# Performance work log

Hardware: AMD Instinct MI355X
Metric: run time of the kernel (lower is better)

The kernel has to match this reference:

```python
import jax, jax.numpy as jnp
import numpy as np

B, L1, Q_DIM, V_DIM = 4, 4096, 256, 256
NH, NL, NP = 8, 4, 4
LEVELS = [(128, 128), (64, 64), (32, 32), (16, 16)]
L2 = sum(h * w for h, w in LEVELS)  # 21760


def setup_inputs() -> dict:
    key = jax.random.key(0)
    ks = jax.random.split(key, 12)
    xav = lambda k, so, si: jax.random.normal(k, (so, si), jnp.float32) * np.sqrt(2.0 / (so + si)).astype(np.float32)
    # reference windows: centers in [0.1,0.9], box sizes in [0.05,0.25]
    c = 0.1 + 0.8 * jax.random.uniform(ks[0], (B, L1, 2), jnp.float32)
    s = 0.05 + 0.2 * jax.random.uniform(ks[1], (B, L1, 2), jnp.float32)
    v_shape = jnp.array(LEVELS, dtype=jnp.int32)
    v_start_index = jnp.array(np.cumsum([0] + [h * w for h, w in LEVELS[:-1]]), dtype=jnp.int32)
    return {
        'query': jax.random.normal(ks[2], (B, L1, Q_DIM), jnp.float32),
        'value': jax.random.normal(ks[3], (B, L2, V_DIM), jnp.float32),
        'v_shape': v_shape,
        'v_mask': jnp.zeros((B, L2), jnp.bool_),
        'v_start_index': v_start_index,
        'v_valid_ratios': jnp.ones((B, 1, 1, NL, 1, 2), jnp.float32),
        'ref_windows': jnp.concatenate([c, s], axis=-1),
        'Wo': 0.01 * jax.random.normal(ks[4], (NH * NL * NP * 2, Q_DIM), jnp.float32),
        'bo': 0.5 * jax.random.normal(ks[5], (NH * NL * NP * 2,), jnp.float32),
        'Wa': 0.02 * jax.random.normal(ks[6], (NH * NL * NP, Q_DIM), jnp.float32),
        'ba': jnp.zeros((NH * NL * NP,), jnp.float32),
        'Wv': xav(ks[7], V_DIM, V_DIM),
        'bv': jnp.zeros((V_DIM,), jnp.float32),
        'Wout': xav(ks[8], Q_DIM, V_DIM),
        'bout': jnp.zeros((Q_DIM,), jnp.float32),
    }


def _ms_deform_sample(value, v_shape, v_start, loc):
    """value: (b,l2,h,d); loc: (b,l1,h,L,P,2) in [0,1] -> (b,l1,L,P,h,d).
    Bilinear sampling with zero padding, align_corners=False semantics."""
    b, l2, h, d = value.shape
    _, l1, _, L, P, _ = loc.shape
    Hi = v_shape[:, 0][None, None, None, :, None]  # (1,1,1,L,1) int
    Wi = v_shape[:, 1][None, None, None, :, None]
    x = loc[..., 0] * Wi.astype(loc.dtype) - 0.5  # (b,l1,h,L,P)
    y = loc[..., 1] * Hi.astype(loc.dtype) - 0.5
    x0 = jnp.floor(x)
    y0 = jnp.floor(y)
    lx, ly = x - x0, y - y0
    x0i = x0.astype(jnp.int32)
    y0i = y0.astype(jnp.int32)
    start = v_start[None, None, None, :, None]
    acc = jnp.zeros((b, l1 * L * P, h, d), loc.dtype)
    for dy, wy in ((0, 1.0 - ly), (1, ly)):
        for dx, wx in ((0, 1.0 - lx), (1, lx)):
            xi = x0i + dx
            yi = y0i + dy
            valid = (xi >= 0) & (xi < Wi) & (yi >= 0) & (yi < Hi)
            w = wx * wy * valid.astype(loc.dtype)  # (b,l1,h,L,P)
            xc = jnp.clip(xi, 0, Wi - 1)
            yc = jnp.clip(yi, 0, Hi - 1)
            flat = start + yc * Wi + xc  # (b,l1,h,L,P) index into l2
            flat_t = flat.transpose(0, 1, 3, 4, 2).reshape(b, l1 * L * P, h)
            w_t = w.transpose(0, 1, 3, 4, 2).reshape(b, l1 * L * P, h)
            g = jnp.take_along_axis(value, flat_t[..., None], axis=1)  # (b,M,h,d)
            acc = acc + g * w_t[..., None]
    return acc.reshape(b, l1, L, P, h, d)


def reference(query, value, v_shape, v_mask, v_start_index, v_valid_ratios, ref_windows,
              Wo, bo, Wa, ba, Wv, bv, Wout, bout):
    b, l1, _ = query.shape
    l2 = value.shape[1]
    hd = value.shape[-1] // NH
    v = value @ Wv.T + bv
    v = jnp.where(v_mask[..., None], 0.0, v).reshape(b, l2, NH, hd)
    off = (query @ Wo.T + bo).reshape(b, l1, NH, NL, NP, 2)
    attn = jax.nn.softmax((query @ Wa.T + ba).reshape(b, l1, NH, NL * NP), axis=-1)
    attn = attn.reshape(b, l1, NH, NL, NP)
    loc = ref_windows[:, :, None, None, None, :2] + off / 8.0 * ref_windows[:, :, None, None, None, 2:]
    loc = loc * v_valid_ratios
    sampled = _ms_deform_sample(v, v_shape, v_start_index, loc)  # (b,l1,L,P,h,d)
    out = jnp.einsum('blLPhd,blhLP->blhd', sampled, attn).reshape(b, l1, NH * hd)
    out = out @ Wout.T + bout
    return out, attn
```

## Files before the change

kernel.cpp:

```cpp
#include <hip/hip_runtime.h>
#include <cstdint>
#include <cstddef>


#define L2_LEN 21760
#define BQ_TOT 16384

typedef __attribute__((ext_vector_type(8))) _Float16 half8;
typedef __attribute__((ext_vector_type(4))) float    f32x4;

__device__ __forceinline__ void glds16(const _Float16* g, _Float16* l) {
    __builtin_amdgcn_global_load_lds(
        (const __attribute__((address_space(1))) void*)g,
        (__attribute__((address_space(3))) void*)l, 16, 0, 0);
}
__device__ __forceinline__ half8 cvt8(float4 a, float4 b) {
    half8 h;
    h[0] = (_Float16)a.x; h[1] = (_Float16)a.y;
    h[2] = (_Float16)a.z; h[3] = (_Float16)a.w;
    h[4] = (_Float16)b.x; h[5] = (_Float16)b.y;
    h[6] = (_Float16)b.z; h[7] = (_Float16)b.w;
    return h;
}

__global__ __launch_bounds__(256) void cvt_weights(
    const float* __restrict__ Wv, const float* __restrict__ Wo,
    const float* __restrict__ Wa, const float* __restrict__ Wout,
    const float* __restrict__ bv, const float* __restrict__ bo,
    const float* __restrict__ ba, const float* __restrict__ bout,
    _Float16* __restrict__ Wp, float* __restrict__ bp)
{
    const int gid = blockIdx.x * 256 + threadIdx.x;
    const float* src; int off8;
    if      (gid <  8192) { src = Wv;   off8 = gid;         }
    else if (gid < 16384) { src = Wo;   off8 = gid -  8192; }
    else if (gid < 20480) { src = Wa;   off8 = gid - 16384; }
    else                  { src = Wout; off8 = gid - 20480; }
    const float4 f0 = ((const float4*)src)[off8 * 2];
    const float4 f1 = ((const float4*)src)[off8 * 2 + 1];
    ((half8*)Wp)[gid] = cvt8(f0, f1);
    if (gid < 896) {
        float b;
        if      (gid < 256) b = bv[gid];
        else if (gid < 512) b = bo[gid - 256];
        else if (gid < 640) b = ba[gid - 512];
        else                b = bout[gid - 640];
        bp[gid] = b;
    }
}

__global__ __launch_bounds__(512) void gemm_vproj(
    const float* __restrict__ A,
    const _Float16* __restrict__ Wp,
    const float* __restrict__ bp,
    _Float16* __restrict__ vh,
    const unsigned char* __restrict__ mask)
{
    __shared__ _Float16 As[4096];
    __shared__ _Float16 Bs[8192];

    const int t = threadIdx.x, lane = t & 63, wid = t >> 6;
    const int wm = wid >> 2, wn = wid & 3;
    const int bm = blockIdx.x;

    const int ar = t >> 2, akp = t & 3;
    const float* Ag = A + (size_t)(bm * 128 + ar) * 256 + akp * 8;
    _Float16* Ad = &As[((ar >> 4) * 64 + akp * 16 + (ar & 15)) * 8];

    const int u0 = wid * 128 + lane, u1 = u0 + 64;
    const int br0 = ((u0 >> 6) << 4) + (u0 & 15), bk0 = ((u0 >> 4) & 3) * 8;
    const int br1 = ((u1 >> 6) << 4) + (u1 & 15), bk1 = ((u1 >> 4) & 3) * 8;
    const _Float16* Wg0 = Wp + (size_t)br0 * 256 + bk0;
    const _Float16* Wg1 = Wp + (size_t)br1 * 256 + bk1;
    _Float16* Bd0 = &Bs[(size_t)wid * 1024];
    _Float16* Bd1 = Bd0 + 512;

    f32x4 acc[4][4] = {};

    for (int kk = 0; kk < 256; kk += 32) {
        const float4 a0 = *(const float4*)(Ag + kk);
        const float4 a1 = *(const float4*)(Ag + kk + 4);
        __syncthreads();
        glds16(Wg0 + kk, Bd0);
        glds16(Wg1 + kk, Bd1);
        *(half8*)Ad = cvt8(a0, a1);
        __syncthreads();
        half8 ah[4], bh[4];
#pragma unroll
        for (int x = 0; x < 4; ++x) {
            ah[x] = ((const half8*)As)[(wm * 4 + x) * 64 + lane];
            bh[x] = ((const half8*)Bs)[(wn * 4 + x) * 64 + lane];
        }
#pragma unroll
        for (int m = 0; m < 4; ++m)
#pragma unroll
            for (int n = 0; n < 4; ++n)
                acc[m][n] = __builtin_amdgcn_mfma_f32_16x16x32_f16(
                    ah[m], bh[n], acc[m][n], 0, 0, 0);
    }

    const int b = bm / 170;
    const int l2b = (bm - b * 170) * 128;
    const int cl = lane & 15, rl = (lane >> 4) * 4;
#pragma unroll
    for (int m = 0; m < 4; ++m) {
        const int ro = wm * 64 + m * 16 + rl;
        float mz[4];
#pragma unroll
        for (int r = 0; r < 4; ++r)
            mz[r] = mask[bm * 128 + ro + r] ? 0.0f : 1.0f;
#pragma unroll
        for (int n = 0; n < 4; ++n) {
            const int col = wn * 64 + n * 16 + cl;
            const int h = col >> 5, c = col & 31;
            const float bb = bp[col];
            _Float16* dst = vh + ((size_t)(b * 8 + h) * L2_LEN + l2b + ro) * 32 + c;
#pragma unroll
            for (int r = 0; r < 4; ++r)
                dst[(size_t)r * 32] = (_Float16)((acc[m][n][r] + bb) * mz[r]);
        }
    }
}

template<bool A_F32>
__global__ __launch_bounds__(256) void gemm_qo(
    const void* __restrict__ Av, const _Float16* __restrict__ Wp,
    const float* __restrict__ bp, int wrow0,
    float* __restrict__ C, int ldC)
{
    __shared__ _Float16 As[4096];
    __shared__ _Float16 Bs[4096];

    const int t = threadIdx.x, lane = t & 63, wid = t >> 6;
    const int wm = wid >> 1, wn = wid & 1;
    const int bm = blockIdx.x, bn = blockIdx.y;

    const int u0 = wid * 128 + lane, u1 = u0 + 64;
    const int br0 = ((u0 >> 6) << 4) + (u0 & 15), bk0 = ((u0 >> 4) & 3) * 8;
    const int br1 = ((u1 >> 6) << 4) + (u1 & 15), bk1 = ((u1 >> 4) & 3) * 8;
    const _Float16* Wg0 = Wp + (size_t)(wrow0 + bn * 128 + br0) * 256 + bk0;
    const _Float16* Wg1 = Wp + (size_t)(wrow0 + bn * 128 + br1) * 256 + bk1;
    _Float16* Bd0 = &Bs[(size_t)wid * 1024];
    _Float16* Bd1 = Bd0 + 512;

    const float*    Agf = nullptr; _Float16* Adf0 = nullptr; _Float16* Adf1 = nullptr;
    const _Float16* Agh0 = nullptr; const _Float16* Agh1 = nullptr;
    _Float16* Adh0 = nullptr; _Float16* Adh1 = nullptr;
    if (A_F32) {
        const int r = t >> 1, kp = (t & 1) * 2;
        Agf  = (const float*)Av + (size_t)(bm * 128 + r) * 256 + kp * 8;
        Adf0 = &As[((r >> 4) * 64 + kp * 16 + (r & 15)) * 8];
        Adf1 = Adf0 + 128;
    } else {
        Agh0 = (const _Float16*)Av + (size_t)(bm * 128 + br0) * 256 + bk0;
        Agh1 = (const _Float16*)Av + (size_t)(bm * 128 + br1) * 256 + bk1;
        Adh0 = &As[(size_t)wid * 1024];
        Adh1 = Adh0 + 512;
    }

    f32x4 acc[4][4] = {};

    for (int kk = 0; kk < 256; kk += 32) {
        float4 a0, a1, a2, a3;
        if (A_F32) {
            a0 = *(const float4*)(Agf + kk);      a1 = *(const float4*)(Agf + kk + 4);
            a2 = *(const float4*)(Agf + kk + 8);  a3 = *(const float4*)(Agf + kk + 12);
        }
        __syncthreads();
        glds16(Wg0 + kk, Bd0);
        glds16(Wg1 + kk, Bd1);
        if (A_F32) {
            *(half8*)Adf0 = cvt8(a0, a1);
            *(half8*)Adf1 = cvt8(a2, a3);
        } else {
            glds16(Agh0 + kk, Adh0);
            glds16(Agh1 + kk, Adh1);
        }
        __syncthreads();
        half8 ah[4], bh[4];
#pragma unroll
        for (int x = 0; x < 4; ++x) {
            ah[x] = ((const half8*)As)[(wm * 4 + x) * 64 + lane];
            bh[x] = ((const half8*)Bs)[(wn * 4 + x) * 64 + lane];
        }
#pragma unroll
        for (int m = 0; m < 4; ++m)
#pragma unroll
            for (int n = 0; n < 4; ++n)
                acc[m][n] = __builtin_amdgcn_mfma_f32_16x16x32_f16(
                    ah[m], bh[n], acc[m][n], 0, 0, 0);
    }

    const int rb = bm * 128 + wm * 64, cb = bn * 128 + wn * 64;
    const int cl = lane & 15, rl = (lane >> 4) * 4;
#pragma unroll
    for (int n = 0; n < 4; ++n) {
        const float bb = bp[wrow0 + cb + n * 16 + cl];
#pragma unroll
        for (int m = 0; m < 4; ++m)
#pragma unroll
            for (int r = 0; r < 4; ++r)
                C[(size_t)(rb + m * 16 + rl + r) * ldC + cb + n * 16 + cl] =
                    acc[m][n][r] + bb;
    }
}

__global__ __launch_bounds__(128) void sample_fused(
    const _Float16* __restrict__ v,
    const float* __restrict__ qp,
    const float* __restrict__ ref,
    const float* __restrict__ vr,
    float* __restrict__ attn_out,
    _Float16* __restrict__ sout)
{
    constexpr int HH[4] = {128, 64, 32, 16};
    constexpr int SS[4] = {0, 16384, 20480, 21504};

    const int t  = threadIdx.x;
    const int q  = blockIdx.x * 4 + (t >> 5);
    const int h  = (t >> 2) & 7;
    const int c0 = (t & 3) * 8;
    const int b  = q >> 12;

    const float* lg = qp + (size_t)q * 384 + 256 + h * 16;
    const float4 l0 = ((const float4*)lg)[0], l1 = ((const float4*)lg)[1];
    const float4 l2 = ((const float4*)lg)[2], l3 = ((const float4*)lg)[3];
    float ap[16] = {l0.x, l0.y, l0.z, l0.w, l1.x, l1.y, l1.z, l1.w,
                    l2.x, l2.y, l2.z, l2.w, l3.x, l3.y, l3.z, l3.w};
    float mx = ap[0];
#pragma unroll
    for (int j = 1; j < 16; ++j) mx = fmaxf(mx, ap[j]);
    float sum = 0.0f;
#pragma unroll
    for (int j = 0; j < 16; ++j) { ap[j] = __expf(ap[j] - mx); sum += ap[j]; }
    const float inv = 1.0f / sum;
#pragma unroll
    for (int j = 0; j < 16; ++j) ap[j] *= inv;
    if (c0 == 0) {
        float4* ao = (float4*)(attn_out + ((size_t)q * 8 + h) * 16);
        ao[0] = make_float4(ap[0], ap[1], ap[2], ap[3]);
        ao[1] = make_float4(ap[4], ap[5], ap[6], ap[7]);
        ao[2] = make_float4(ap[8], ap[9], ap[10], ap[11]);
        ao[3] = make_float4(ap[12], ap[13], ap[14], ap[15]);
    }

    const float4 rw = *(const float4*)(ref + (size_t)q * 4);
    const float* op = qp + (size_t)q * 384 + h * 32;

    float acc[8] = {};

#pragma unroll
    for (int l = 0; l < 4; ++l) {
        const int HW = HH[l];
        const float fHW = (float)HW;
        const float vrx = vr[(b * 4 + l) * 2 + 0];
        const float vry = vr[(b * 4 + l) * 2 + 1];
        const _Float16* vb = v + ((size_t)(b * 8 + h) * L2_LEN + SS[l]) * 32 + c0;
#pragma unroll
        for (int p = 0; p < 4; ++p) {
            const float a  = ap[l * 4 + p];
            const float ox = op[(l * 4 + p) * 2 + 0];
            const float oy = op[(l * 4 + p) * 2 + 1];
            const float x = (rw.x + ox * 0.125f * rw.z) * vrx * fHW - 0.5f;
            const float y = (rw.y + oy * 0.125f * rw.w) * vry * fHW - 0.5f;
            const float x0f = floorf(x), y0f = floorf(y);
            const float fx = x - x0f, fy = y - y0f;
            const int x0 = (int)x0f, y0 = (int)y0f;
            const float wx0 = (x0 >= 0 && x0 < HW)         ? (1.0f - fx) : 0.0f;
            const float wx1 = (x0 + 1 >= 0 && x0 + 1 < HW) ? fx          : 0.0f;
            const float wy0 = (y0 >= 0 && y0 < HW)         ? (1.0f - fy) : 0.0f;
            const float wy1 = (y0 + 1 >= 0 && y0 + 1 < HW) ? fy          : 0.0f;
            const int xc0 = min(max(x0, 0), HW - 1), xc1 = min(max(x0 + 1, 0), HW - 1);
            const int yc0 = min(max(y0, 0), HW - 1), yc1 = min(max(y0 + 1, 0), HW - 1);
            const float w00 = wx0 * wy0 * a, w01 = wx1 * wy0 * a;
            const float w10 = wx0 * wy1 * a, w11 = wx1 * wy1 * a;
            const half8 g00 = *(const half8*)(vb + (size_t)(yc0 * HW + xc0) * 32);
            const half8 g01 = *(const half8*)(vb + (size_t)(yc0 * HW + xc1) * 32);
            const half8 g10 = *(const half8*)(vb + (size_t)(yc1 * HW + xc0) * 32);
            const half8 g11 = *(const half8*)(vb + (size_t)(yc1 * HW + xc1) * 32);
#pragma unroll
            for (int j = 0; j < 8; ++j)
                acc[j] += w00 * (float)g00[j] + w01 * (float)g01[j]
                        + w10 * (float)g10[j] + w11 * (float)g11[j];
        }
    }

    half8 o;
#pragma unroll
    for (int j = 0; j < 8; ++j) o[j] = (_Float16)acc[j];
    *(half8*)(sout + (size_t)q * 256 + h * 32 + c0) = o;
}

extern "C" void kernel_launch(void* const* d_in, const int* in_sizes, int n_in,
                              void* d_out, int out_size, void* d_ws, size_t ws_size,
                              hipStream_t stream)
{
    const float*         query    = (const float*)d_in[0];
    const float*         value    = (const float*)d_in[1];
    const unsigned char* v_mask   = (const unsigned char*)d_in[3];
    const float*         v_ratios = (const float*)d_in[5];
    const float*         ref_w    = (const float*)d_in[6];
    const float*         Wo       = (const float*)d_in[7];
    const float*         bo       = (const float*)d_in[8];
    const float*         Wa       = (const float*)d_in[9];
    const float*         ba       = (const float*)d_in[10];
    const float*         Wv       = (const float*)d_in[11];
    const float*         bv       = (const float*)d_in[12];
    const float*         Wout     = (const float*)d_in[13];
    const float*         bout     = (const float*)d_in[14];

    float* out      = (float*)d_out;
    float* attn_out = out + (size_t)BQ_TOT * 256;

    _Float16* Wp = (_Float16*)d_ws;
    float*    bp = (float*)(Wp + 896 * 256);
    float*    qp = bp + 896;
    _Float16* vh = (_Float16*)(qp + (size_t)BQ_TOT * 384);
    _Float16* Sf = vh + (size_t)4 * L2_LEN * 256;

    cvt_weights<<<112, 256, 0, stream>>>(Wv, Wo, Wa, Wout, bv, bo, ba, bout, Wp, bp);
    gemm_vproj<<<680, 512, 0, stream>>>(value, Wp, bp, vh, v_mask);
    gemm_qo<true><<<dim3(128, 3), 256, 0, stream>>>(query, Wp, bp, 256, qp, 384);
    sample_fused<<<4096, 128, 0, stream>>>(vh, qp, ref_w, v_ratios, attn_out, Sf);
    gemm_qo<false><<<dim3(128, 2), 256, 0, stream>>>(Sf, Wp, bp, 640, out, 256);
}
```

Before: 274.5 us.

## Double-buffer GEMMs, drop weight pre-conversion, repartition sampling by level with fdot2

The separate weight-conversion kernel is removed. GEMMs now read fp32 weights and convert them while staging to shared memory. All GEMMs become register-prefetched, double-buffered loops with XOR-swizzled LDS layouts, swapped MFMA operands for vectorized epilogue stores, and 2-D grids for the value projection. The sampling kernel now assigns one level per lane instead of one channel slice, loads full 32-channel rows, and accumulates with packed fp16 dot products. Results are combined across lanes with shuffles. This lowers bilinear weight precision to fp16 and raises register pressure.

```diff
diff --git a/kernel.cpp b/kernel.cpp
--- a/kernel.cpp
+++ b/kernel.cpp
@@ -7,6 +7,8 @@
 #define BQ_TOT 16384
 
 typedef __attribute__((ext_vector_type(8))) _Float16 half8;
+typedef __attribute__((ext_vector_type(4))) _Float16 half4;
+typedef __attribute__((ext_vector_type(2))) _Float16 half2v;
 typedef __attribute__((ext_vector_type(4))) float    f32x4;
 
 __device__ __forceinline__ void glds16(const _Float16* g, _Float16* l) {
@@ -22,186 +24,201 @@
     h[6] = (_Float16)b.z; h[7] = (_Float16)b.w;
     return h;
 }
-
-__global__ __launch_bounds__(256) void cvt_weights(
-    const float* __restrict__ Wv, const float* __restrict__ Wo,
-    const float* __restrict__ Wa, const float* __restrict__ Wout,
-    const float* __restrict__ bv, const float* __restrict__ bo,
-    const float* __restrict__ ba, const float* __restrict__ bout,
-    _Float16* __restrict__ Wp, float* __restrict__ bp)
+__device__ __forceinline__ int swz_chunk(int c) {
+    const int frag = c >> 6, r = (c >> 2) & 15, k = c & 3;
+    return (frag * 64 + ((k * 16 + r) ^ (k << 2))) * 8;
+}
+
+__global__ __launch_bounds__(256, 3) void gemm_vproj(
+    const float* __restrict__ A, const float* __restrict__ Wv,
+    const float* __restrict__ bv, const unsigned char* __restrict__ mask,
+    _Float16* __restrict__ vh)
 {
-    const int gid = blockIdx.x * 256 + threadIdx.x;
-    const float* src; int off8;
-    if      (gid <  8192) { src = Wv;   off8 = gid;         }
-    else if (gid < 16384) { src = Wo;   off8 = gid -  8192; }
-    else if (gid < 20480) { src = Wa;   off8 = gid - 16384; }
-    else                  { src = Wout; off8 = gid - 20480; }
-    const float4 f0 = ((const float4*)src)[off8 * 2];
-    const float4 f1 = ((const float4*)src)[off8 * 2 + 1];
-    ((half8*)Wp)[gid] = cvt8(f0, f1);
-    if (gid < 896) {
-        float b;
-        if      (gid < 256) b = bv[gid];
-        else if (gid < 512) b = bo[gid - 256];
-        else if (gid < 640) b = ba[gid - 512];
-        else                b = bout[gid - 640];
-        bp[gid] = b;
-    }
-}
-
-__global__ __launch_bounds__(512) void gemm_vproj(
-    const float* __restrict__ A,
-    const _Float16* __restrict__ Wp,
-    const float* __restrict__ bp,
-    _Float16* __restrict__ vh,
-    const unsigned char* __restrict__ mask)
-{
-    __shared__ _Float16 As[4096];
-    __shared__ _Float16 Bs[8192];
-
-    const int t = threadIdx.x, lane = t & 63, wid = t >> 6;
-    const int wm = wid >> 2, wn = wid & 3;
-    const int bm = blockIdx.x;
-
-    const int ar = t >> 2, akp = t & 3;
-    const float* Ag = A + (size_t)(bm * 128 + ar) * 256 + akp * 8;
-    _Float16* Ad = &As[((ar >> 4) * 64 + akp * 16 + (ar & 15)) * 8];
-
-    const int u0 = wid * 128 + lane, u1 = u0 + 64;
-    const int br0 = ((u0 >> 6) << 4) + (u0 & 15), bk0 = ((u0 >> 4) & 3) * 8;
-    const int br1 = ((u1 >> 6) << 4) + (u1 & 15), bk1 = ((u1 >> 4) & 3) * 8;
-    const _Float16* Wg0 = Wp + (size_t)br0 * 256 + bk0;
-    const _Float16* Wg1 = Wp + (size_t)br1 * 256 + bk1;
-    _Float16* Bd0 = &Bs[(size_t)wid * 1024];
-    _Float16* Bd1 = Bd0 + 512;
-
-    f32x4 acc[4][4] = {};
-
-    for (int kk = 0; kk < 256; kk += 32) {
-        const float4 a0 = *(const float4*)(Ag + kk);
-        const float4 a1 = *(const float4*)(Ag + kk + 4);
-        __syncthreads();
-        glds16(Wg0 + kk, Bd0);
-        glds16(Wg1 + kk, Bd1);
-        *(half8*)Ad = cvt8(a0, a1);
-        __syncthreads();
-        half8 ah[4], bh[4];
-#pragma unroll
-        for (int x = 0; x < 4; ++x) {
-            ah[x] = ((const half8*)As)[(wm * 4 + x) * 64 + lane];
-            bh[x] = ((const half8*)Bs)[(wn * 4 + x) * 64 + lane];
-        }
-#pragma unroll
-        for (int m = 0; m < 4; ++m)
-#pragma unroll
-            for (int n = 0; n < 4; ++n)
-                acc[m][n] = __builtin_amdgcn_mfma_f32_16x16x32_f16(
-                    ah[m], bh[n], acc[m][n], 0, 0, 0);
-    }
-
-    const int b = bm / 170;
-    const int l2b = (bm - b * 170) * 128;
-    const int cl = lane & 15, rl = (lane >> 4) * 4;
-#pragma unroll
-    for (int m = 0; m < 4; ++m) {
-        const int ro = wm * 64 + m * 16 + rl;
-        float mz[4];
-#pragma unroll
-        for (int r = 0; r < 4; ++r)
-            mz[r] = mask[bm * 128 + ro + r] ? 0.0f : 1.0f;
-#pragma unroll
-        for (int n = 0; n < 4; ++n) {
-            const int col = wn * 64 + n * 16 + cl;
-            const int h = col >> 5, c = col & 31;
-            const float bb = bp[col];
-            _Float16* dst = vh + ((size_t)(b * 8 + h) * L2_LEN + l2b + ro) * 32 + c;
-#pragma unroll
-            for (int r = 0; r < 4; ++r)
-                dst[(size_t)r * 32] = (_Float16)((acc[m][n][r] + bb) * mz[r]);
-        }
-    }
-}
-
-template<bool A_F32>
-__global__ __launch_bounds__(256) void gemm_qo(
-    const void* __restrict__ Av, const _Float16* __restrict__ Wp,
-    const float* __restrict__ bp, int wrow0,
-    float* __restrict__ C, int ldC)
-{
-    __shared__ _Float16 As[4096];
-    __shared__ _Float16 Bs[4096];
+    __shared__ _Float16 As[2][4096];
+    __shared__ _Float16 Bs[2][4096];
 
     const int t = threadIdx.x, lane = t & 63, wid = t >> 6;
     const int wm = wid >> 1, wn = wid & 1;
     const int bm = blockIdx.x, bn = blockIdx.y;
 
-    const int u0 = wid * 128 + lane, u1 = u0 + 64;
-    const int br0 = ((u0 >> 6) << 4) + (u0 & 15), bk0 = ((u0 >> 4) & 3) * 8;
-    const int br1 = ((u1 >> 6) << 4) + (u1 & 15), bk1 = ((u1 >> 4) & 3) * 8;
-    const _Float16* Wg0 = Wp + (size_t)(wrow0 + bn * 128 + br0) * 256 + bk0;
-    const _Float16* Wg1 = Wp + (size_t)(wrow0 + bn * 128 + br1) * 256 + bk1;
-    _Float16* Bd0 = &Bs[(size_t)wid * 1024];
-    _Float16* Bd1 = Bd0 + 512;
-
-    const float*    Agf = nullptr; _Float16* Adf0 = nullptr; _Float16* Adf1 = nullptr;
-    const _Float16* Agh0 = nullptr; const _Float16* Agh1 = nullptr;
-    _Float16* Adh0 = nullptr; _Float16* Adh1 = nullptr;
-    if (A_F32) {
-        const int r = t >> 1, kp = (t & 1) * 2;
-        Agf  = (const float*)Av + (size_t)(bm * 128 + r) * 256 + kp * 8;
-        Adf0 = &As[((r >> 4) * 64 + kp * 16 + (r & 15)) * 8];
-        Adf1 = Adf0 + 128;
-    } else {
-        Agh0 = (const _Float16*)Av + (size_t)(bm * 128 + br0) * 256 + bk0;
-        Agh1 = (const _Float16*)Av + (size_t)(bm * 128 + br1) * 256 + bk1;
-        Adh0 = &As[(size_t)wid * 1024];
-        Adh1 = Adh0 + 512;
-    }
+    const int r0 = t >> 2, kg = (t & 3) * 8;
+    const float* Ag0 = A  + ((size_t)(bm * 128) + r0) * 256 + kg;
+    const float* Ag1 = Ag0 + (size_t)64 * 256;
+    const float* Bg0 = Wv + ((size_t)(bn * 128) + r0) * 256 + kg;
+    const float* Bg1 = Bg0 + (size_t)64 * 256;
+    const int d0 = swz_chunk(t), d1 = swz_chunk(t + 256);
+    const int rsw = (lane ^ ((lane >> 4) << 2)) * 8;
 
     f32x4 acc[4][4] = {};
-
-    for (int kk = 0; kk < 256; kk += 32) {
-        float4 a0, a1, a2, a3;
-        if (A_F32) {
-            a0 = *(const float4*)(Agf + kk);      a1 = *(const float4*)(Agf + kk + 4);
-            a2 = *(const float4*)(Agf + kk + 8);  a3 = *(const float4*)(Agf + kk + 12);
-        }
-        __syncthreads();
-        glds16(Wg0 + kk, Bd0);
-        glds16(Wg1 + kk, Bd1);
-        if (A_F32) {
-            *(half8*)Adf0 = cvt8(a0, a1);
-            *(half8*)Adf1 = cvt8(a2, a3);
-        } else {
-            glds16(Agh0 + kk, Adh0);
-            glds16(Agh1 + kk, Adh1);
-        }
-        __syncthreads();
+    float4 pa0, pa1, pa2, pa3, pb0, pb1, pb2, pb3;
+
+    pa0 = *(const float4*)Ag0; pa1 = *(const float4*)(Ag0 + 4);
+    pa2 = *(const float4*)Ag1; pa3 = *(const float4*)(Ag1 + 4);
+    pb0 = *(const float4*)Bg0; pb1 = *(const float4*)(Bg0 + 4);
+    pb2 = *(const float4*)Bg1; pb3 = *(const float4*)(Bg1 + 4);
+    *(half8*)&As[0][d0] = cvt8(pa0, pa1); *(half8*)&As[0][d1] = cvt8(pa2, pa3);
+    *(half8*)&Bs[0][d0] = cvt8(pb0, pb1); *(half8*)&Bs[0][d1] = cvt8(pb2, pb3);
+    __syncthreads();
+
+    for (int it = 0; it < 8; ++it) {
+        const int cur = it & 1;
+        if (it < 7) {
+            const int kk = (it + 1) * 32;
+            pa0 = *(const float4*)(Ag0 + kk); pa1 = *(const float4*)(Ag0 + kk + 4);
+            pa2 = *(const float4*)(Ag1 + kk); pa3 = *(const float4*)(Ag1 + kk + 4);
+            pb0 = *(const float4*)(Bg0 + kk); pb1 = *(const float4*)(Bg0 + kk + 4);
+            pb2 = *(const float4*)(Bg1 + kk); pb3 = *(const float4*)(Bg1 + kk + 4);
+        }
         half8 ah[4], bh[4];
 #pragma unroll
         for (int x = 0; x < 4; ++x) {
-            ah[x] = ((const half8*)As)[(wm * 4 + x) * 64 + lane];
-            bh[x] = ((const half8*)Bs)[(wn * 4 + x) * 64 + lane];
+            ah[x] = *(const half8*)&As[cur][(wm * 4 + x) * 512 + rsw];
+            bh[x] = *(const half8*)&Bs[cur][(wn * 4 + x) * 512 + rsw];
         }
 #pragma unroll
         for (int m = 0; m < 4; ++m)
 #pragma unroll
             for (int n = 0; n < 4; ++n)
                 acc[m][n] = __builtin_amdgcn_mfma_f32_16x16x32_f16(
-                    ah[m], bh[n], acc[m][n], 0, 0, 0);
-    }
-
-    const int rb = bm * 128 + wm * 64, cb = bn * 128 + wn * 64;
+                    bh[n], ah[m], acc[m][n], 0, 0, 0);
+        if (it < 7) {
+            *(half8*)&As[cur ^ 1][d0] = cvt8(pa0, pa1);
+            *(half8*)&As[cur ^ 1][d1] = cvt8(pa2, pa3);
+            *(half8*)&Bs[cur ^ 1][d0] = cvt8(pb0, pb1);
+            *(half8*)&Bs[cur ^ 1][d1] = cvt8(pb2, pb3);
+        }
+        __syncthreads();
+    }
+
     const int cl = lane & 15, rl = (lane >> 4) * 4;
-#pragma unroll
-    for (int n = 0; n < 4; ++n) {
-        const float bb = bp[wrow0 + cb + n * 16 + cl];
+    const int b = bm / 170;
+#pragma unroll
+    for (int m = 0; m < 4; ++m) {
+        const int row = bm * 128 + wm * 64 + m * 16 + cl;
+        const float mz = mask[row] ? 0.0f : 1.0f;
+        const int l2i = row - b * L2_LEN;
+#pragma unroll
+        for (int n = 0; n < 4; ++n) {
+            const int col = bn * 128 + wn * 64 + n * 16 + rl;
+            const float4 bb = *(const float4*)(bv + col);
+            const int h = col >> 5, c = col & 31;
+            half4 o;
+            o[0] = (_Float16)((acc[m][n][0] + bb.x) * mz);
+            o[1] = (_Float16)((acc[m][n][1] + bb.y) * mz);
+            o[2] = (_Float16)((acc[m][n][2] + bb.z) * mz);
+            o[3] = (_Float16)((acc[m][n][3] + bb.w) * mz);
+            *(half4*)(vh + ((size_t)(b * 8 + h) * L2_LEN + l2i) * 32 + c) = o;
+        }
+    }
+}
+
+template<bool A_F16>
+__global__ __launch_bounds__(256, 3) void gemm_qo(
+    const void* __restrict__ Av,
+    const float* __restrict__ W0, const float* __restrict__ W1,
+    const float* __restrict__ b0, const float* __restrict__ b1, int n_split,
+    float* __restrict__ C, int ldC)
+{
+    __shared__ _Float16 As[2][4096];
+    __shared__ _Float16 Bs[2][4096];
+
+    const int t = threadIdx.x, lane = t & 63, wid = t >> 6;
+    const int wm = wid >> 1, wn = wid & 1;
+    const int bm = blockIdx.x, bn = blockIdx.y;
+
+    const int cb = bn * 128;
+    const float* Wt; const float* bt;
+    if (cb < n_split) { Wt = W0 + (size_t)cb * 256;             bt = b0 + cb; }
+    else              { Wt = W1 + (size_t)(cb - n_split) * 256; bt = b1 + (cb - n_split); }
+
+    const int r0 = t >> 2, kg = (t & 3) * 8;
+    const float* Bg0 = Wt + ((size_t)r0) * 256 + kg;
+    const float* Bg1 = Bg0 + (size_t)64 * 256;
+    const int d0 = swz_chunk(t), d1 = swz_chunk(t + 256);
+    const int rsw = (lane ^ ((lane >> 4) << 2)) * 8;
+
+    const float* Agf0 = nullptr; const float* Agf1 = nullptr;
+    const _Float16* Agh0 = nullptr; const _Float16* Agh1 = nullptr;
+    _Float16* AdH0 = nullptr; _Float16* AdH1 = nullptr;
+    if (A_F16) {
+        const int u0 = wid * 128 + lane, u1 = u0 + 64;
+        const int ar0 = ((u0 >> 6) << 4) + (u0 & 15), ak0 = ((u0 >> 4) & 3) * 8;
+        const int ar1 = ((u1 >> 6) << 4) + (u1 & 15), ak1 = ((u1 >> 4) & 3) * 8;
+        Agh0 = (const _Float16*)Av + ((size_t)(bm * 128) + ar0) * 256 + ak0;
+        Agh1 = (const _Float16*)Av + ((size_t)(bm * 128) + ar1) * 256 + ak1;
+        AdH0 = (_Float16*)&As[0][0] + wid * 1024;
+        AdH1 = AdH0 + 512;
+    } else {
+        Agf0 = (const float*)Av + ((size_t)(bm * 128) + r0) * 256 + kg;
+        Agf1 = Agf0 + (size_t)64 * 256;
+    }
+
+    f32x4 acc[4][4] = {};
+    float4 pa0, pa1, pa2, pa3, pb0, pb1, pb2, pb3;
+
+    pb0 = *(const float4*)Bg0; pb1 = *(const float4*)(Bg0 + 4);
+    pb2 = *(const float4*)Bg1; pb3 = *(const float4*)(Bg1 + 4);
+    if (A_F16) { glds16(Agh0, AdH0); glds16(Agh1, AdH1); }
+    else {
+        pa0 = *(const float4*)Agf0; pa1 = *(const float4*)(Agf0 + 4);
+        pa2 = *(const float4*)Agf1; pa3 = *(const float4*)(Agf1 + 4);
+        *(half8*)&As[0][d0] = cvt8(pa0, pa1);
+        *(half8*)&As[0][d1] = cvt8(pa2, pa3);
+    }
+    *(half8*)&Bs[0][d0] = cvt8(pb0, pb1);
+    *(half8*)&Bs[0][d1] = cvt8(pb2, pb3);
+    __syncthreads();
+
+    for (int it = 0; it < 8; ++it) {
+        const int cur = it & 1;
+        if (it < 7) {
+            const int kk = (it + 1) * 32;
+            if (A_F16) {
+                glds16(Agh0 + kk, AdH0 + (cur ^ 1) * 4096);
+                glds16(Agh1 + kk, AdH1 + (cur ^ 1) * 4096);
+            } else {
+                pa0 = *(const float4*)(Agf0 + kk); pa1 = *(const float4*)(Agf0 + kk + 4);
+                pa2 = *(const float4*)(Agf1 + kk); pa3 = *(const float4*)(Agf1 + kk + 4);
+            }
+            pb0 = *(const float4*)(Bg0 + kk); pb1 = *(const float4*)(Bg0 + kk + 4);
+            pb2 = *(const float4*)(Bg1 + kk); pb3 = *(const float4*)(Bg1 + kk + 4);
+        }
+        half8 ah[4], bh[4];
+#pragma unroll
+        for (int x = 0; x < 4; ++x) {
+            ah[x] = *(const half8*)&As[cur][(wm * 4 + x) * 512 + (A_F16 ? lane * 8 : rsw)];
+            bh[x] = *(const half8*)&Bs[cur][(wn * 4 + x) * 512 + rsw];
+        }
 #pragma unroll
         for (int m = 0; m < 4; ++m)
 #pragma unroll
-            for (int r = 0; r < 4; ++r)
-                C[(size_t)(rb + m * 16 + rl + r) * ldC + cb + n * 16 + cl] =
-                    acc[m][n][r] + bb;
+            for (int n = 0; n < 4; ++n)
+                acc[m][n] = __builtin_amdgcn_mfma_f32_16x16x32_f16(
+                    bh[n], ah[m], acc[m][n], 0, 0, 0);
+        if (it < 7) {
+            if (!A_F16) {
+                *(half8*)&As[cur ^ 1][d0] = cvt8(pa0, pa1);
+                *(half8*)&As[cur ^ 1][d1] = cvt8(pa2, pa3);
+            }
+            *(half8*)&Bs[cur ^ 1][d0] = cvt8(pb0, pb1);
+            *(half8*)&Bs[cur ^ 1][d1] = cvt8(pb2, pb3);
+        }
+        __syncthreads();
+    }
+
+    const int cl = lane & 15, rl = (lane >> 4) * 4;
+#pragma unroll
+    for (int m = 0; m < 4; ++m) {
+        const int row = bm * 128 + wm * 64 + m * 16 + cl;
+#pragma unroll
+        for (int n = 0; n < 4; ++n) {
+            const int co = wn * 64 + n * 16 + rl;
+            const float4 bb = *(const float4*)(bt + co);
+            float4 r;
+            r.x = acc[m][n][0] + bb.x; r.y = acc[m][n][1] + bb.y;
+            r.z = acc[m][n][2] + bb.z; r.w = acc[m][n][3] + bb.w;
+            *(float4*)(C + (size_t)row * ldC + cb + co) = r;
+        }
     }
 }
 
@@ -209,86 +226,122 @@
     const _Float16* __restrict__ v,
     const float* __restrict__ qp,
     const float* __restrict__ ref,
-    const float* __restrict__ vr,
+    const float* __restrict__ vrp,
     float* __restrict__ attn_out,
     _Float16* __restrict__ sout)
 {
-    constexpr int HH[4] = {128, 64, 32, 16};
-    constexpr int SS[4] = {0, 16384, 20480, 21504};
-
     const int t  = threadIdx.x;
     const int q  = blockIdx.x * 4 + (t >> 5);
     const int h  = (t >> 2) & 7;
-    const int c0 = (t & 3) * 8;
+    const int lv = t & 3;
     const int b  = q >> 12;
 
     const float* lg = qp + (size_t)q * 384 + 256 + h * 16;
     const float4 l0 = ((const float4*)lg)[0], l1 = ((const float4*)lg)[1];
     const float4 l2 = ((const float4*)lg)[2], l3 = ((const float4*)lg)[3];
-    float ap[16] = {l0.x, l0.y, l0.z, l0.w, l1.x, l1.y, l1.z, l1.w,
-                    l2.x, l2.y, l2.z, l2.w, l3.x, l3.y, l3.z, l3.w};
-    float mx = ap[0];
-#pragma unroll
-    for (int j = 1; j < 16; ++j) mx = fmaxf(mx, ap[j]);
+    float e[16] = {l0.x, l0.y, l0.z, l0.w, l1.x, l1.y, l1.z, l1.w,
+                   l2.x, l2.y, l2.z, l2.w, l3.x, l3.y, l3.z, l3.w};
+    float mx = e[0];
+#pragma unroll
+    for (int j = 1; j < 16; ++j) mx = fmaxf(mx, e[j]);
     float sum = 0.0f;
 #pragma unroll
-    for (int j = 0; j < 16; ++j) { ap[j] = __expf(ap[j] - mx); sum += ap[j]; }
+    for (int j = 0; j < 16; ++j) { e[j] = __expf(e[j] - mx); sum += e[j]; }
     const float inv = 1.0f / sum;
-#pragma unroll
-    for (int j = 0; j < 16; ++j) ap[j] *= inv;
-    if (c0 == 0) {
-        float4* ao = (float4*)(attn_out + ((size_t)q * 8 + h) * 16);
-        ao[0] = make_float4(ap[0], ap[1], ap[2], ap[3]);
-        ao[1] = make_float4(ap[4], ap[5], ap[6], ap[7]);
-        ao[2] = make_float4(ap[8], ap[9], ap[10], ap[11]);
-        ao[3] = make_float4(ap[12], ap[13], ap[14], ap[15]);
-    }
+    float aw[4];
+#pragma unroll
+    for (int p = 0; p < 4; ++p) aw[p] = e[lv * 4 + p] * inv;
+    *(float4*)(attn_out + ((size_t)q * 8 + h) * 16 + lv * 4) =
+        make_float4(aw[0], aw[1], aw[2], aw[3]);
 
     const float4 rw = *(const float4*)(ref + (size_t)q * 4);
-    const float* op = qp + (size_t)q * 384 + h * 32;
-
-    float acc[8] = {};
-
-#pragma unroll
-    for (int l = 0; l < 4; ++l) {
-        const int HW = HH[l];
-        const float fHW = (float)HW;
-        const float vrx = vr[(b * 4 + l) * 2 + 0];
-        const float vry = vr[(b * 4 + l) * 2 + 1];
-        const _Float16* vb = v + ((size_t)(b * 8 + h) * L2_LEN + SS[l]) * 32 + c0;
-#pragma unroll
-        for (int p = 0; p < 4; ++p) {
-            const float a  = ap[l * 4 + p];
-            const float ox = op[(l * 4 + p) * 2 + 0];
-            const float oy = op[(l * 4 + p) * 2 + 1];
-            const float x = (rw.x + ox * 0.125f * rw.z) * vrx * fHW - 0.5f;
-            const float y = (rw.y + oy * 0.125f * rw.w) * vry * fHW - 0.5f;
-            const float x0f = floorf(x), y0f = floorf(y);
-            const float fx = x - x0f, fy = y - y0f;
-            const int x0 = (int)x0f, y0 = (int)y0f;
-            const float wx0 = (x0 >= 0 && x0 < HW)         ? (1.0f - fx) : 0.0f;
-            const float wx1 = (x0 + 1 >= 0 && x0 + 1 < HW) ? fx          : 0.0f;
-            const float wy0 = (y0 >= 0 && y0 < HW)         ? (1.0f - fy) : 0.0f;
-            const float wy1 = (y0 + 1 >= 0 && y0 + 1 < HW) ? fy          : 0.0f;
-            const int xc0 = min(max(x0, 0), HW - 1), xc1 = min(max(x0 + 1, 0), HW - 1);
-            const int yc0 = min(max(y0, 0), HW - 1), yc1 = min(max(y0 + 1, 0), HW - 1);
-            const float w00 = wx0 * wy0 * a, w01 = wx1 * wy0 * a;
-            const float w10 = wx0 * wy1 * a, w11 = wx1 * wy1 * a;
-            const half8 g00 = *(const half8*)(vb + (size_t)(yc0 * HW + xc0) * 32);
-            const half8 g01 = *(const half8*)(vb + (size_t)(yc0 * HW + xc1) * 32);
-            const half8 g10 = *(const half8*)(vb + (size_t)(yc1 * HW + xc0) * 32);
-            const half8 g11 = *(const half8*)(vb + (size_t)(yc1 * HW + xc1) * 32);
-#pragma unroll
-            for (int j = 0; j < 8; ++j)
-                acc[j] += w00 * (float)g00[j] + w01 * (float)g01[j]
-                        + w10 * (float)g10[j] + w11 * (float)g11[j];
-        }
-    }
-
+    const float* op = qp + (size_t)q * 384 + h * 32 + lv * 8;
+    const float4 o01 = ((const float4*)op)[0], o23 = ((const float4*)op)[1];
+    const float oxv[4] = {o01.x, o01.z, o23.x, o23.z};
+    const float oyv[4] = {o01.y, o01.w, o23.y, o23.w};
+
+    const int HW = 128 >> lv;
+    constexpr int SS[4] = {0, 16384, 20480, 21504};
+    const int start = SS[0] * 0 + (lv == 0 ? 0 : (lv == 1 ? 16384 : (lv == 2 ? 20480 : 21504)));
+    const float fHW = (float)HW;
+    const float vrx = vrp[(b * 4 + lv) * 2 + 0];
+    const float vry = vrp[(b * 4 + lv) * 2 + 1];
+    const _Float16* vb = v + ((size_t)(b * 8 + h) * L2_LEN + start) * 32;
+
+    float acc[32] = {};
+
+#pragma unroll
+    for (int p = 0; p < 4; ++p) {
+        const float a = aw[p];
+        const float x = (rw.x + oxv[p] * 0.125f * rw.z) * vrx * fHW - 0.5f;
+        const float y = (rw.y + oyv[p] * 0.125f * rw.w) * vry * fHW - 0.5f;
+        const float x0f = floorf(x), y0f = floorf(y);
+        const float fx = x - x0f, fy = y - y0f;
+        const int x0 = (int)x0f, y0 = (int)y0f;
+        const float wx0 = (x0 >= 0 && x0 < HW)         ? (1.0f - fx) : 0.0f;
+        const float wx1 = (x0 + 1 >= 0 && x0 + 1 < HW) ? fx          : 0.0f;
+        const float wy0 = (y0 >= 0 && y0 < HW)         ? (1.0f - fy) : 0.0f;
+        const float wy1 = (y0 + 1 >= 0 && y0 + 1 < HW) ? fy          : 0.0f;
+        const int xc0 = min(max(x0, 0), HW - 1), xc1 = min(max(x0 + 1, 0), HW - 1);
+        const int yc0 = min(max(y0, 0), HW - 1), yc1 = min(max(y0 + 1, 0), HW - 1);
+        half2v wA, wB;
+        wA[0] = (_Float16)(wx0 * wy0 * a); wA[1] = (_Float16)(wx1 * wy0 * a);
+        wB[0] = (_Float16)(wx0 * wy1 * a); wB[1] = (_Float16)(wx1 * wy1 * a);
+
+        const uint4* p00 = (const uint4*)(vb + (size_t)(yc0 * HW + xc0) * 32);
+        const uint4* p01 = (const uint4*)(vb + (size_t)(yc0 * HW + xc1) * 32);
+        const uint4* p10 = (const uint4*)(vb + (size_t)(yc1 * HW + xc0) * 32);
+        const uint4* p11 = (const uint4*)(vb + (size_t)(yc1 * HW + xc1) * 32);
+        unsigned u00[16], u01[16], u10[16], u11[16];
+#pragma unroll
+        for (int i = 0; i < 4; ++i) {
+            *(uint4*)&u00[i * 4] = p00[i];
+            *(uint4*)&u01[i * 4] = p01[i];
+            *(uint4*)&u10[i * 4] = p10[i];
+            *(uint4*)&u11[i * 4] = p11[i];
+        }
+#pragma unroll
+        for (int d = 0; d < 16; ++d) {
+            const unsigned loA = __builtin_amdgcn_perm(u00[d], u01[d], 0x01000504u);
+            const unsigned hiA = __builtin_amdgcn_perm(u00[d], u01[d], 0x03020706u);
+            const unsigned loB = __builtin_amdgcn_perm(u10[d], u11[d], 0x01000504u);
+            const unsigned hiB = __builtin_amdgcn_perm(u10[d], u11[d], 0x03020706u);
+#if __has_builtin(__builtin_amdgcn_fdot2)
+            acc[2 * d]     = __builtin_amdgcn_fdot2(__builtin_bit_cast(half2v, loA), wA, acc[2 * d], false);
+            acc[2 * d]     = __builtin_amdgcn_fdot2(__builtin_bit_cast(half2v, loB), wB, acc[2 * d], false);
+            acc[2 * d + 1] = __builtin_amdgcn_fdot2(__builtin_bit_cast(half2v, hiA), wA, acc[2 * d + 1], false);
+            acc[2 * d + 1] = __builtin_amdgcn_fdot2(__builtin_bit_cast(half2v, hiB), wB, acc[2 * d + 1], false);
+#else
+            const half2v xA = __builtin_bit_cast(half2v, loA), yA = __builtin_bit_cast(half2v, hiA);
+            const half2v xB = __builtin_bit_cast(half2v, loB), yB = __builtin_bit_cast(half2v, hiB);
+            acc[2 * d]     += (float)xA[0] * (float)wA[0] + (float)xA[1] * (float)wA[1]
+                            + (float)xB[0] * (float)wB[0] + (float)xB[1] * (float)wB[1];
+            acc[2 * d + 1] += (float)yA[0] * (float)wA[0] + (float)yA[1] * (float)wA[1]
+                            + (float)yB[0] * (float)wB[0] + (float)yB[1] * (float)wB[1];
+#endif
+        }
+    }
+
+    float t1[32];
+#pragma unroll
+    for (int j = 0; j < 32; ++j) t1[j] = __shfl_xor(acc[j], 1);
+    float r16[16];
+#pragma unroll
+    for (int j = 0; j < 16; ++j)
+        r16[j] = (lv & 1) ? (acc[16 + j] + t1[16 + j]) : (acc[j] + t1[j]);
+    float t2[16];
+#pragma unroll
+    for (int j = 0; j < 16; ++j) t2[j] = __shfl_xor(r16[j], 2);
+    float r8[8];
+#pragma unroll
+    for (int j = 0; j < 8; ++j)
+        r8[j] = (lv & 2) ? (r16[8 + j] + t2[8 + j]) : (r16[j] + t2[j]);
+
+    const int cq = ((lv & 1) << 4) | ((lv & 2) << 2);
     half8 o;
 #pragma unroll
-    for (int j = 0; j < 8; ++j) o[j] = (_Float16)acc[j];
-    *(half8*)(sout + (size_t)q * 256 + h * 32 + c0) = o;
+    for (int j = 0; j < 8; ++j) o[j] = (_Float16)r8[j];
+    *(half8*)(sout + (size_t)q * 256 + h * 32 + cq) = o;
 }
 
 extern "C" void kernel_launch(void* const* d_in, const int* in_sizes, int n_in,
@@ -312,15 +365,14 @@
     float* out      = (float*)d_out;
     float* attn_out = out + (size_t)BQ_TOT * 256;
 
-    _Float16* Wp = (_Float16*)d_ws;
-    float*    bp = (float*)(Wp + 896 * 256);
-    float*    qp = bp + 896;
+    float*    qp = (float*)d_ws;
     _Float16* vh = (_Float16*)(qp + (size_t)BQ_TOT * 384);
     _Float16* Sf = vh + (size_t)4 * L2_LEN * 256;
 
-    cvt_weights<<<112, 256, 0, stream>>>(Wv, Wo, Wa, Wout, bv, bo, ba, bout, Wp, bp);
-    gemm_vproj<<<680, 512, 0, stream>>>(value, Wp, bp, vh, v_mask);
-    gemm_qo<true><<<dim3(128, 3), 256, 0, stream>>>(query, Wp, bp, 256, qp, 384);
+    gemm_vproj<<<dim3(680, 2), 256, 0, stream>>>(value, Wv, bv, v_mask, vh);
+    gemm_qo<false><<<dim3(128, 3), 256, 0, stream>>>(
+        query, Wo, Wa, bo, ba, 256, qp, 384);
     sample_fused<<<4096, 128, 0, stream>>>(vh, qp, ref_w, v_ratios, attn_out, Sf);
-    gemm_qo<false><<<dim3(128, 2), 256, 0, stream>>>(Sf, Wp, bp, 640, out, 256);
-}
+    gemm_qo<true><<<dim3(128, 2), 256, 0, stream>>>(
+        Sf, Wout, Wout, bout, bout, 256, out, 256);
+}
```

After: 309.9 us. 1.13x slower.
